# Optimization experiments

Hardware: AMD Instinct MI355X
Metric: run time of the kernel (lower is better)

Reference implementation:

```python
import jax, jax.numpy as jnp
import numpy as np

EMBED_DIM = 128
NUM_SYMBOLS = 200000
PAD = NUM_SYMBOLS
B = 1024          # query batch
FEW = 5           # support set size
NB = 200          # neighbors per entity (fixed by module docstring)
D_MODEL = 2 * EMBED_DIM       # 256
D_INNER = 2 * D_MODEL         # 512
HID = 2 * D_MODEL             # LSTMCell hidden = 2*input_dim = 512
STEPS = 4                     # process_steps
LN_EPS = 1e-5


def setup_inputs() -> dict:
    key = jax.random.key(0)
    ks = jax.random.split(key, 16)

    def conn(k, n):
        c = jax.random.randint(k, (n, NB, 2), 0, NUM_SYMBOLS, dtype=jnp.int64)
        # pad last 50 neighbor slots so the masked max-pool path is exercised
        return c.at[:, 150:, :].set(PAD)

    inp = {
        "query_left_connections": conn(ks[0], B),
        "query_right_connections": conn(ks[1], B),
        "support_left_connections": conn(ks[2], FEW),
        "support_right_connections": conn(ks[3], FEW),
        "query_left_degrees": jax.random.randint(ks[4], (B,), 1, NB, dtype=jnp.int32),
        "query_right_degrees": jax.random.randint(ks[5], (B,), 1, NB, dtype=jnp.int32),
        "support_left_degrees": jax.random.randint(ks[6], (FEW,), 1, NB, dtype=jnp.int32),
        "support_right_degrees": jax.random.randint(ks[7], (FEW,), 1, NB, dtype=jnp.int32),
    }

    # parameters (eval mode: dropout disabled)
    emb = jax.random.normal(ks[8], (NUM_SYMBOLS + 1, EMBED_DIM), jnp.float32) * 0.02
    inp["emb"] = emb.at[PAD].set(0.0)              # padding_idx row is zero
    inp["gcn_W"] = jax.random.normal(ks[9], (EMBED_DIM, 2 * EMBED_DIM), jnp.float32) * 0.05
    inp["gcn_wb"] = jnp.zeros((EMBED_DIM,), jnp.float32)   # gcn_w linear bias
    inp["gcn_b"] = jnp.zeros((EMBED_DIM,), jnp.float32)    # extra gcn_b param (init constant 0)
    inp["proj1_W"] = jax.random.normal(ks[10], (D_INNER, D_MODEL), jnp.float32) * 0.05
    inp["proj1_b"] = jnp.zeros((D_INNER,), jnp.float32)
    inp["proj2_W"] = jax.random.normal(ks[11], (D_MODEL, D_INNER), jnp.float32) * 0.05
    inp["proj2_b"] = jnp.zeros((D_MODEL,), jnp.float32)
    inp["ln_g"] = jnp.ones((D_MODEL,), jnp.float32)
    inp["ln_b"] = jnp.zeros((D_MODEL,), jnp.float32)
    inp["W_ih"] = jax.random.normal(ks[12], (4 * HID, D_MODEL), jnp.float32) * 0.04
    inp["W_hh"] = jax.random.normal(ks[13], (4 * HID, HID), jnp.float32) * 0.04
    inp["b_ih"] = jnp.zeros((4 * HID,), jnp.float32)
    inp["b_hh"] = jnp.zeros((4 * HID,), jnp.float32)
    return inp


def _neighbor_encoder(conn, emb, gcn_W, gcn_wb, gcn_b):
    # conn: (n, NB, 2) ints; gather embed + concat + linear + leaky_relu + masked max + tanh
    rel, ent = conn[:, :, 0], conn[:, :, 1]
    pad_mask = (rel == PAD) | (ent == PAD)                      # (n, NB)
    x = jnp.concatenate([emb[rel], emb[ent]], axis=-1)          # (n, NB, 2E)
    p = jnp.einsum('nke,de->nkd', x, gcn_W) + gcn_wb + gcn_b    # (n, NB, E)
    p = jax.nn.leaky_relu(p, negative_slope=0.1)
    p = jnp.where(pad_mask[:, :, None], -jnp.inf, p)
    return jnp.tanh(jnp.max(p, axis=1))                         # (n, E)


def _support_encoder(x, p1W, p1b, p2W, p2b, g, b):
    # FFN with residual + LayerNorm (GMatching SupportEncoder), dropout off in eval
    h = jax.nn.relu(x @ p1W.T + p1b)
    o = h @ p2W.T + p2b + x
    mu = jnp.mean(o, axis=-1, keepdims=True)
    var = jnp.var(o, axis=-1, keepdims=True)
    return (o - mu) / jnp.sqrt(var + LN_EPS) * g + b


def _query_encoder(support, query, W_ih, W_hh, b_ih, b_hh):
    # GMatching QueryEncoder: LSTMCell attention, `process_steps` iterations
    # support: (1, D_MODEL), query: (bq, D_MODEL)
    bq = query.shape[0]
    h_r = jnp.zeros((bq, HID), query.dtype)
    c = jnp.zeros((bq, HID), query.dtype)
    h = query
    for _ in range(STEPS):
        gates = query @ W_ih.T + b_ih + h_r @ W_hh.T + b_hh     # (bq, 4*HID)
        i, f, g, o = jnp.split(gates, 4, axis=-1)
        c = jax.nn.sigmoid(f) * c + jax.nn.sigmoid(i) * jnp.tanh(g)
        h_new = jax.nn.sigmoid(o) * jnp.tanh(c)                 # (bq, HID)
        h = query + h_new[:, :D_MODEL]
        attn = jax.nn.softmax(h @ support.T, axis=1)            # (bq, 1)
        r = attn @ support                                      # (bq, D_MODEL)
        h_r = jnp.concatenate([h, r], axis=1)
    return h


def reference(query_left_connections, query_right_connections,
              support_left_connections, support_right_connections,
              query_left_degrees, query_right_degrees,
              support_left_degrees, support_right_degrees,
              emb, gcn_W, gcn_wb, gcn_b,
              proj1_W, proj1_b, proj2_W, proj2_b, ln_g, ln_b,
              W_ih, W_hh, b_ih, b_hh):
    ql = _neighbor_encoder(query_left_connections, emb, gcn_W, gcn_wb, gcn_b)
    qr = _neighbor_encoder(query_right_connections, emb, gcn_W, gcn_wb, gcn_b)
    sl = _neighbor_encoder(support_left_connections, emb, gcn_W, gcn_wb, gcn_b)
    sr = _neighbor_encoder(support_right_connections, emb, gcn_W, gcn_wb, gcn_b)
    query_neighbor = jnp.concatenate([ql, qr], axis=-1)      # (B, D_MODEL)
    support_neighbor = jnp.concatenate([sl, sr], axis=-1)    # (FEW, D_MODEL)

    support_g = _support_encoder(support_neighbor[None], proj1_W, proj1_b, proj2_W, proj2_b, ln_g, ln_b)
    support_g = jnp.mean(support_g, axis=1)                  # (1, D_MODEL)
    query_g = _support_encoder(query_neighbor[:, None, :], proj1_W, proj1_b, proj2_W, proj2_b, ln_g, ln_b)
    query_g = query_g[:, 0, :]                               # (B, D_MODEL)

    query_f = _query_encoder(support_g, query_g, W_ih, W_hh, b_ih, b_hh)  # (B, D_MODEL)
    return (query_f @ support_g.T)[:, 0]                     # (B,)
```

## Files before the change

### kernel.cpp

```cpp
#include <hip/hip_runtime.h>
#include <math.h>

#define EMBED   128
#define DMODEL  256
#define DINNER  512
#define HIDN    512
#define NBK     200
#define BQ      1024
#define FEW     5
#define PAD_IDX 200000
#define LN_EPS  1e-5f
#define NTILES  7

#define EMB_ELEMS 25600128
#define EMB_THREADS (EMB_ELEMS / 8)
#define EMB_BLOCKS ((EMB_THREADS + 255) / 256)

typedef short          s16x8  __attribute__((ext_vector_type(8)));
typedef float          f32x4  __attribute__((ext_vector_type(4)));
typedef float          f32x16 __attribute__((ext_vector_type(16)));
typedef unsigned int   u32;
typedef unsigned short u16;

__device__ __forceinline__ float sigmoidf_(float x) { return 1.0f / (1.0f + expf(-x)); }

__device__ __forceinline__ u32 f2bf(float f) {
    u32 u = __builtin_bit_cast(u32, f);
    u += 0x7fffu + ((u >> 16) & 1u);
    return u >> 16;
}
__device__ __forceinline__ s16x8 pack8(float4 a, float4 b) {
    typedef u32 u32x4_ __attribute__((ext_vector_type(4)));
    u32x4_ q;
    q.x = f2bf(a.x) | (f2bf(a.y) << 16);
    q.y = f2bf(a.z) | (f2bf(a.w) << 16);
    q.z = f2bf(b.x) | (f2bf(b.y) << 16);
    q.w = f2bf(b.z) | (f2bf(b.w) << 16);
    return __builtin_bit_cast(s16x8, q);
}

__global__ __launch_bounds__(256) void convert_all_kernel(
    const float* __restrict__ W_ih, const float* __restrict__ W_hh,
    const float* __restrict__ p1W,  const float* __restrict__ p2W,
    const float* __restrict__ emb,
    u16* __restrict__ wih_bf, u16* __restrict__ whh_bf,
    u16* __restrict__ p1_bf,  u16* __restrict__ p2_bf,
    u16* __restrict__ emb_bf)
{
    int bid = blockIdx.x;
    if (bid >= 384) {
        size_t gid = (size_t)(bid - 384) * 256 + threadIdx.x;
        if (gid < EMB_THREADS) {
            size_t base = gid * 8;
            float4 x0 = *(const float4*)(emb + base);
            float4 x1 = *(const float4*)(emb + base + 4);
            *(s16x8*)(emb_bf + base) = pack8(x0, x1);
        }
        return;
    }
    int gid = bid * 256 + threadIdx.x;
    const float* src; u16* dst; int local, stride, KS, liveRemap;
    if (gid < 32768)      { local = gid;          src = W_ih; dst = wih_bf; stride = 256; KS = 8;  liveRemap = 1; }
    else if (gid < 65536) { local = gid - 32768;  src = W_hh; dst = whh_bf; stride = 512; KS = 8;  liveRemap = 1; }
    else if (gid < 81920) { local = gid - 65536;  src = p1W;  dst = p1_bf;  stride = 256; KS = 8;  liveRemap = 0; }
    else                  { local = gid - 81920;  src = p2W;  dst = p2_bf;  stride = 512; KS = 16; liveRemap = 0; }
    int lane = local & 63;
    int ts   = local >> 6;
    int ks   = ts & (KS - 1);
    int tile = ts / KS;
    int n  = tile * 16 + (lane & 15);
    int kb = ks * 32 + (lane >> 4) * 8;
    int row = liveRemap ? ((n >> 8) * 512 + (n & 255)) : n;
    const float* sp = src + (size_t)row * stride + kb;
    float4 x0 = *(const float4*)sp;
    float4 x1 = *(const float4*)(sp + 4);
    *(s16x8*)(dst + (size_t)local * 8) = pack8(x0, x1);
}

template<bool BF>
__global__ __launch_bounds__(256) void neighbor_kernel(
    const int* __restrict__ qlc, const int* __restrict__ qrc,
    const int* __restrict__ slc, const int* __restrict__ src_,
    const float* __restrict__ emb, const u16* __restrict__ emb_bf,
    const float* __restrict__ W,
    const float* __restrict__ wb,  const float* __restrict__ bb,
    float* __restrict__ qn, float* __restrict__ sn)
{
    int b = blockIdx.x;
    const int* conn; float* out; int n; int side;
    if (b < BQ)                { conn = qlc;  n = b;            side = 0; out = qn; }
    else if (b < 2*BQ)         { conn = qrc;  n = b - BQ;       side = 1; out = qn; }
    else if (b < 2*BQ + FEW)   { conn = slc;  n = b - 2*BQ;     side = 0; out = sn; }
    else                       { conn = src_; n = b - 2*BQ-FEW; side = 1; out = sn; }

    int t = threadIdx.x;
    int w = t >> 6, l = t & 63;
    int d0 = w * 32;
    int m31 = l & 31, half = l >> 5;

    s16x8 afrag[16];
    const float* wrow = W + (d0 + m31) * DMODEL + half * 8;
    #pragma unroll
    for (int ks = 0; ks < 16; ++ks) {
        float4 x0 = *(const float4*)(wrow + ks * 16);
        float4 x1 = *(const float4*)(wrow + ks * 16 + 4);
        afrag[ks] = pack8(x0, x1);
    }

    const int2* crow = (const int2*)(conn + n * NBK * 2);
    int srel[NTILES], sent[NTILES];
    u32 vmask = 0;
    #pragma unroll
    for (int nt = 0; nt < NTILES; ++nt) {
        int krow = nt * 32 + m31;
        int rel = PAD_IDX, ent = PAD_IDX;
        if (krow < NBK) { int2 re = crow[krow]; rel = re.x; ent = re.y; }
        int v = (rel != PAD_IDX) && (ent != PAD_IDX);
        if (v) vmask |= (1u << nt);
        srel[nt] = v ? rel : PAD_IDX;
        sent[nt] = v ? ent : PAD_IDX;
    }

    float vm[16];
    #pragma unroll
    for (int r = 0; r < 16; ++r) vm[r] = -INFINITY;

    for (int nt = 0; nt < NTILES; ++nt) {
        if (!__any((int)((vmask >> nt) & 1u))) continue;

        s16x8 bfr[16];
        if (BF) {
            const u16* pr = emb_bf + (size_t)srel[nt] * EMBED + half * 8;
            const u16* pe = emb_bf + (size_t)sent[nt] * EMBED + half * 8;
            #pragma unroll
            for (int ks = 0; ks < 8; ++ks) bfr[ks]     = *(const s16x8*)(pr + ks * 16);
            #pragma unroll
            for (int ks = 0; ks < 8; ++ks) bfr[8 + ks] = *(const s16x8*)(pe + ks * 16);
        } else {
            const float* pr = emb + (size_t)srel[nt] * EMBED + half * 8;
            const float* pe = emb + (size_t)sent[nt] * EMBED + half * 8;
            #pragma unroll
            for (int ks = 0; ks < 8; ++ks)
                bfr[ks] = pack8(*(const float4*)(pr + ks * 16), *(const float4*)(pr + ks * 16 + 4));
            #pragma unroll
            for (int ks = 0; ks < 8; ++ks)
                bfr[8 + ks] = pack8(*(const float4*)(pe + ks * 16), *(const float4*)(pe + ks * 16 + 4));
        }

        f32x16 acc = {0.f,0.f,0.f,0.f,0.f,0.f,0.f,0.f,0.f,0.f,0.f,0.f,0.f,0.f,0.f,0.f};
        #pragma unroll
        for (int j = 0; j < 16; ++j)
            acc = __builtin_amdgcn_mfma_f32_32x32x16_bf16(afrag[j], bfr[j], acc, 0, 0, 0);

        int cv = (vmask >> nt) & 1;
        #pragma unroll
        for (int r = 0; r < 16; ++r) {
            float v = cv ? acc[r] : -INFINITY;
            vm[r] = fmaxf(vm[r], v);
        }
    }

    #pragma unroll
    for (int off = 1; off < 32; off <<= 1) {
        #pragma unroll
        for (int r = 0; r < 16; ++r)
            vm[r] = fmaxf(vm[r], __shfl_xor(vm[r], off, 64));
    }

    if (m31 == 0) {
        #pragma unroll
        for (int r = 0; r < 16; ++r) {
            int d = d0 + (r & 3) + 8 * (r >> 2) + 4 * half;
            float p = vm[r] + wb[d] + bb[d];
            p = (p >= 0.f) ? p : 0.1f * p;
            out[n * DMODEL + side * EMBED + d] = tanhf(p);
        }
    }
}

__global__ __launch_bounds__(512) void support_enc_kernel(
    const float* __restrict__ qn, const float* __restrict__ sn,
    const u16* __restrict__ p1_bf, const float* __restrict__ p1b,
    const u16* __restrict__ p2_bf, const float* __restrict__ p2b,
    const float* __restrict__ lng, const float* __restrict__ lnb,
    float* __restrict__ query_g, float* __restrict__ sup_ln)
{
    __shared__ __align__(16) float xs[16][260];
    __shared__ __align__(16) float hsd[16][516];
    __shared__ __align__(16) float os[16][260];
    int t = threadIdx.x;
    int w = t >> 6, l = t & 63;
    int r0 = blockIdx.x * 16;

    #pragma unroll
    for (int j = 0; j < 8; ++j) {
        int idx = j * 512 + t;
        int r = idx >> 8, cc = idx & 255;
        int row = r0 + r;
        float v = 0.f;
        if (row < BQ + FEW)
            v = (row < BQ) ? qn[(size_t)row * DMODEL + cc] : sn[(size_t)(row - BQ) * DMODEL + cc];
        xs[r][cc] = v;
    }
    __syncthreads();

    int am = l & 15, ak = (l >> 4) * 8;

    s16x8 a1[8];
    #pragma unroll
    for (int ks = 0; ks < 8; ++ks) {
        float4 x0 = *(const float4*)&xs[am][ks * 32 + ak];
        float4 x1 = *(const float4*)&xs[am][ks * 32 + ak + 4];
        a1[ks] = pack8(x0, x1);
    }

    #pragma unroll
    for (int j = 0; j < 4; ++j) {
        int nt = w * 4 + j;
        f32x4 acc = {0.f, 0.f, 0.f, 0.f};
        const u16* bp = p1_bf + (size_t)nt * 4096 + l * 8;
        #pragma unroll
        for (int ks = 0; ks < 8; ++ks) {
            s16x8 bf = *(const s16x8*)(bp + ks * 512);
            acc = __builtin_amdgcn_mfma_f32_16x16x32_bf16(a1[ks], bf, acc, 0, 0, 0);
        }
        int nn = nt * 16 + (l & 15);
        float bj = p1b[nn];
        #pragma unroll
        for (int reg = 0; reg < 4; ++reg) {
            int m = (l >> 4) * 4 + reg;
            hsd[m][nn] = fmaxf(acc[reg] + bj, 0.f);
        }
    }
    __syncthreads();

    s16x8 a2[16];
    #pragma unroll
    for (int ks = 0; ks < 16; ++ks) {
        float4 x0 = *(const float4*)&hsd[am][ks * 32 + ak];
        float4 x1 = *(const float4*)&hsd[am][ks * 32 + ak + 4];
        a2[ks] = pack8(x0, x1);
    }

    #pragma unroll
    for (int j = 0; j < 2; ++j) {
        int nt = w * 2 + j;
        f32x4 acc = {0.f, 0.f, 0.f, 0.f};
        const u16* bp = p2_bf + (size_t)nt * 8192 + l * 8;
        #pragma unroll
        for (int ks = 0; ks < 16; ++ks) {
            s16x8 bf = *(const s16x8*)(bp + ks * 512);
            acc = __builtin_amdgcn_mfma_f32_16x16x32_bf16(a2[ks], bf, acc, 0, 0, 0);
        }
        int nn = nt * 16 + (l & 15);
        float bj = p2b[nn];
        #pragma unroll
        for (int reg = 0; reg < 4; ++reg) {
            int m = (l >> 4) * 4 + reg;
            os[m][nn] = acc[reg] + bj + xs[m][nn];
        }
    }
    __syncthreads();

    for (int j = 0; j < 2; ++j) {
        int m = w * 2 + j;
        float sum = 0.f, sq = 0.f;
        #pragma unroll
        for (int i = 0; i < 4; ++i) {
            float v = os[m][l + 64 * i];
            sum += v; sq += v * v;
        }
        for (int off = 32; off; off >>= 1) {
            sum += __shfl_xor(sum, off, 64);
            sq  += __shfl_xor(sq,  off, 64);
        }
        float mu  = sum * (1.f / DMODEL);
        float var = sq * (1.f / DMODEL) - mu * mu;
        float inv = rsqrtf(var + LN_EPS);
        int row = r0 + m;
        if (row < BQ + FEW) {
            float* outp = (row < BQ) ? (query_g + (size_t)row * DMODEL) : (sup_ln + (size_t)(row - BQ) * DMODEL);
            #pragma unroll
            for (int i = 0; i < 4; ++i) {
                int dd = l + 64 * i;
                outp[dd] = (os[m][dd] - mu) * inv * lng[dd] + lnb[dd];
            }
        }
    }
}

__global__ __launch_bounds__(256) void sWp_kernel(
    const float* __restrict__ sup_ln, const float* __restrict__ W_hh,
    float* __restrict__ sWp)
{
    int w = threadIdx.x >> 6, l = threadIdx.x & 63;
    int wave_id = blockIdx.x * 4 + w;
    float se[4];
    #pragma unroll
    for (int j = 0; j < 4; ++j) {
        float a = 0.f;
        for (int i = 0; i < FEW; ++i) a += sup_ln[i * DMODEL + l + 64 * j];
        se[j] = a * (1.f / FEW);
    }
    for (int i = 0; i < 4; ++i) {
        int p = wave_id * 4 + i;
        int pp = p >> 8, q = p & 255;
        const float* wr = W_hh + (size_t)(pp * 512 + q) * HIDN + 256;
        float part = 0.f;
        #pragma unroll
        for (int j = 0; j < 4; ++j) part += se[j] * wr[l + 64 * j];
        for (int off = 32; off; off >>= 1) part += __shfl_xor(part, off, 64);
        if (l == 0) sWp[p] = part;
    }
}

__global__ __launch_bounds__(512) void lstm_mfma_kernel(
    const float* __restrict__ query_g, const float* __restrict__ sup_ln,
    const float* __restrict__ sWp, const u16* __restrict__ wih_bf,
    const u16* __restrict__ whh_bf, const float* __restrict__ b_ih,
    const float* __restrict__ b_hh, float* __restrict__ out)
{
    __shared__ __align__(16) float qs[16][260];
    __shared__ __align__(16) float hs[16][260];
    __shared__ float sv[DMODEL];
    int t = threadIdx.x;
    int w = t >> 6, l = t & 63;
    int n0 = blockIdx.x * 16;

    if (t < DMODEL) {
        float a = 0.f;
        for (int i = 0; i < FEW; ++i) a += sup_ln[i * DMODEL + t];
        sv[t] = a * (1.f / FEW);
    }
    #pragma unroll
    for (int j = 0; j < 8; ++j) {
        int idx = j * 512 + t;
        int r = idx >> 8, cc = idx & 255;
        qs[r][cc] = query_g[(size_t)(n0 + r) * DMODEL + cc];
    }
    __syncthreads();

    int am = l & 15, ak = (l >> 4) * 8;

    s16x8 af[8];
    #pragma unroll
    for (int ks = 0; ks < 8; ++ks) {
        float4 x0 = *(const float4*)&qs[am][ks * 32 + ak];
        float4 x1 = *(const float4*)&qs[am][ks * 32 + ak + 4];
        af[ks] = pack8(x0, x1);
    }

    f32x4 base[4][2];
    #pragma unroll
    for (int pp = 0; pp < 4; ++pp) {
        #pragma unroll
        for (int qt = 0; qt < 2; ++qt) {
            int tp = pp * 16 + 2 * w + qt;
            f32x4 acc = {0.f, 0.f, 0.f, 0.f};
            const u16* bp = wih_bf + (size_t)tp * 4096 + l * 8;
            #pragma unroll
            for (int ks = 0; ks < 8; ++ks) {
                s16x8 bf = *(const s16x8*)(bp + ks * 512);
                acc = __builtin_amdgcn_mfma_f32_16x16x32_bf16(af[ks], bf, acc, 0, 0, 0);
            }
            base[pp][qt] = acc;
        }
    }
    #pragma unroll
    for (int pp = 0; pp < 4; ++pp) {
        #pragma unroll
        for (int qt = 0; qt < 2; ++qt) {
            int q = w * 32 + qt * 16 + (l & 15);
            float bsv = b_ih[pp * 512 + q] + b_hh[pp * 512 + q];
            base[pp][qt].x += bsv; base[pp][qt].y += bsv;
            base[pp][qt].z += bsv; base[pp][qt].w += bsv;
        }
    }

    float c[2][4];
    #pragma unroll
    for (int qt = 0; qt < 2; ++qt) {
        int q = w * 32 + qt * 16 + (l & 15);
        #pragma unroll
        for (int reg = 0; reg < 4; ++reg) {
            int m = (l >> 4) * 4 + reg;
            float gi = base[0][qt][reg];
            float gg = base[2][qt][reg];
            float go = base[3][qt][reg];
            float cc = sigmoidf_(gi) * tanhf(gg);
            c[qt][reg] = cc;
            hs[m][q] = qs[m][q] + sigmoidf_(go) * tanhf(cc);
        }
    }
    #pragma unroll
    for (int pp = 0; pp < 4; ++pp) {
        #pragma unroll
        for (int qt = 0; qt < 2; ++qt) {
            int q = w * 32 + qt * 16 + (l & 15);
            float sw = sWp[pp * 256 + q];
            base[pp][qt].x += sw; base[pp][qt].y += sw;
            base[pp][qt].z += sw; base[pp][qt].w += sw;
        }
    }
    __syncthreads();

    for (int st = 1; st < 4; ++st) {
        #pragma unroll
        for (int ks = 0; ks < 8; ++ks) {
            float4 x0 = *(const float4*)&hs[am][ks * 32 + ak];
            float4 x1 = *(const float4*)&hs[am][ks * 32 + ak + 4];
            af[ks] = pack8(x0, x1);
        }
        __syncthreads();

        f32x4 gacc[4][2];
        #pragma unroll
        for (int pp = 0; pp < 4; ++pp) {
            #pragma unroll
            for (int qt = 0; qt < 2; ++qt) {
                int tp = pp * 16 + 2 * w + qt;
                f32x4 acc = base[pp][qt];
                const u16* bp = whh_bf + (size_t)tp * 4096 + l * 8;
                #pragma unroll
                for (int ks = 0; ks < 8; ++ks) {
                    s16x8 bf = *(const s16x8*)(bp + ks * 512);
                    acc = __builtin_amdgcn_mfma_f32_16x16x32_bf16(af[ks], bf, acc, 0, 0, 0);
                }
                gacc[pp][qt] = acc;
            }
        }
        #pragma unroll
        for (int qt = 0; qt < 2; ++qt) {
            int q = w * 32 + qt * 16 + (l & 15);
            #pragma unroll
            for (int reg = 0; reg < 4; ++reg) {
                int m = (l >> 4) * 4 + reg;
                float gi = gacc[0][qt][reg];
                float gf = gacc[1][qt][reg];
                float gg = gacc[2][qt][reg];
                float go = gacc[3][qt][reg];
                float cc = sigmoidf_(gf) * c[qt][reg] + sigmoidf_(gi) * tanhf(gg);
                c[qt][reg] = cc;
                hs[m][q] = qs[m][q] + sigmoidf_(go) * tanhf(cc);
            }
        }
        __syncthreads();
    }

    for (int j = 0; j < 2; ++j) {
        int m = w * 2 + j;
        float part = 0.f;
        #pragma unroll
        for (int i = 0; i < 4; ++i) {
            int e = l + 64 * i;
            part += hs[m][e] * sv[e];
        }
        for (int off = 32; off; off >>= 1) part += __shfl_xor(part, off, 64);
        if (l == 0) out[n0 + m] = part;
    }
}

extern "C" void kernel_launch(void* const* d_in, const int* in_sizes, int n_in,
                              void* d_out, int out_size, void* d_ws, size_t ws_size,
                              hipStream_t stream)
{
    const int*   qlc  = (const int*)d_in[0];
    const int*   qrc  = (const int*)d_in[1];
    const int*   slc  = (const int*)d_in[2];
    const int*   src_ = (const int*)d_in[3];
    const float* emb   = (const float*)d_in[8];
    const float* gcnW  = (const float*)d_in[9];
    const float* gcnwb = (const float*)d_in[10];
    const float* gcnb  = (const float*)d_in[11];
    const float* p1W   = (const float*)d_in[12];
    const float* p1b   = (const float*)d_in[13];
    const float* p2W   = (const float*)d_in[14];
    const float* p2b   = (const float*)d_in[15];
    const float* lng   = (const float*)d_in[16];
    const float* lnb   = (const float*)d_in[17];
    const float* W_ih  = (const float*)d_in[18];
    const float* W_hh  = (const float*)d_in[19];
    const float* b_ih  = (const float*)d_in[20];
    const float* b_hh  = (const float*)d_in[21];
    float* out = (float*)d_out;

    char* ws = (char*)d_ws;
    float* qn      = (float*)(ws + 0);
    float* sn      = (float*)(ws + 1048576);
    float* query_g = (float*)(ws + 1053696);
    float* sup_ln  = (float*)(ws + 2102272);
    float* sWp     = (float*)(ws + 2107392);
    u16*   wih_bf  = (u16*)(ws + 2111488);
    u16*   whh_bf  = (u16*)(ws + 2635776);
    u16*   p1_bf   = (u16*)(ws + 3160064);
    u16*   p2_bf   = (u16*)(ws + 3422208);
    u16*   emb_bf  = (u16*)(ws + 3684352);
    (void)in_sizes; (void)n_in; (void)out_size;

    bool have_emb = ws_size >= (size_t)3684352 + (size_t)EMB_ELEMS * 2;
    int grid_conv = 384 + (have_emb ? EMB_BLOCKS : 0);

    convert_all_kernel<<<grid_conv, 256, 0, stream>>>(
        W_ih, W_hh, p1W, p2W, emb, wih_bf, whh_bf, p1_bf, p2_bf, emb_bf);
    if (have_emb)
        neighbor_kernel<true><<<2 * BQ + 2 * FEW, 256, 0, stream>>>(
            qlc, qrc, slc, src_, emb, emb_bf, gcnW, gcnwb, gcnb, qn, sn);
    else
        neighbor_kernel<false><<<2 * BQ + 2 * FEW, 256, 0, stream>>>(
            qlc, qrc, slc, src_, emb, emb_bf, gcnW, gcnwb, gcnb, qn, sn);
    support_enc_kernel<<<(BQ + FEW + 15) / 16, 512, 0, stream>>>(
        qn, sn, p1_bf, p1b, p2_bf, p2b, lng, lnb, query_g, sup_ln);
    sWp_kernel<<<64, 256, 0, stream>>>(sup_ln, W_hh, sWp);
    lstm_mfma_kernel<<<BQ / 16, 512, 0, stream>>>(
        query_g, sup_ln, sWp, wih_bf, whh_bf, b_ih, b_hh, out);
}
```

Before: 404.4 us.

## Stage neighbor embeddings in swizzled LDS and fold support term into LSTM GEMM

In the neighbor kernel, embedding rows are now gathered cooperatively (four threads per row) into a swizzled shared-memory tile, with the next tile prefetched into registers. This replaces per-lane strided gathers that each pulled half-rows. The sWp kernel is removed. The LSTM recurrent GEMM now runs over the full 512-wide hidden input [h, support], with the support vector stored in shared memory and W_hh converted at full width. This drops one launch, but it doubles the recurrent MFMA work and the W_hh conversion, and it adds barriers to the neighbor loop.

```diff
diff --git a/kernel.cpp b/kernel.cpp
--- a/kernel.cpp
+++ b/kernel.cpp
@@ -48,8 +48,8 @@
     u16* __restrict__ emb_bf)
 {
     int bid = blockIdx.x;
-    if (bid >= 384) {
-        size_t gid = (size_t)(bid - 384) * 256 + threadIdx.x;
+    if (bid >= 512) {
+        size_t gid = (size_t)(bid - 512) * 256 + threadIdx.x;
         if (gid < EMB_THREADS) {
             size_t base = gid * 8;
             float4 x0 = *(const float4*)(emb + base);
@@ -60,10 +60,10 @@
     }
     int gid = bid * 256 + threadIdx.x;
     const float* src; u16* dst; int local, stride, KS, liveRemap;
-    if (gid < 32768)      { local = gid;          src = W_ih; dst = wih_bf; stride = 256; KS = 8;  liveRemap = 1; }
-    else if (gid < 65536) { local = gid - 32768;  src = W_hh; dst = whh_bf; stride = 512; KS = 8;  liveRemap = 1; }
-    else if (gid < 81920) { local = gid - 65536;  src = p1W;  dst = p1_bf;  stride = 256; KS = 8;  liveRemap = 0; }
-    else                  { local = gid - 81920;  src = p2W;  dst = p2_bf;  stride = 512; KS = 16; liveRemap = 0; }
+    if (gid < 32768)       { local = gid;          src = W_ih; dst = wih_bf; stride = 256; KS = 8;  liveRemap = 1; }
+    else if (gid < 98304)  { local = gid - 32768;  src = W_hh; dst = whh_bf; stride = 512; KS = 16; liveRemap = 1; }
+    else if (gid < 114688) { local = gid - 98304;  src = p1W;  dst = p1_bf;  stride = 256; KS = 8;  liveRemap = 0; }
+    else                   { local = gid - 114688; src = p2W;  dst = p2_bf;  stride = 512; KS = 16; liveRemap = 0; }
     int lane = local & 63;
     int ts   = local >> 6;
     int ks   = ts & (KS - 1);
@@ -98,6 +98,8 @@
     int d0 = w * 32;
     int m31 = l & 31, half = l >> 5;
 
+    __shared__ __align__(16) u16 bs[64 * 128];
+
     s16x8 afrag[16];
     const float* wrow = W + (d0 + m31) * DMODEL + half * 8;
     #pragma unroll
@@ -108,56 +110,92 @@
     }
 
     const int2* crow = (const int2*)(conn + n * NBK * 2);
-    int srel[NTILES], sent[NTILES];
     u32 vmask = 0;
     #pragma unroll
     for (int nt = 0; nt < NTILES; ++nt) {
         int krow = nt * 32 + m31;
+        if (krow < NBK) {
+            int2 re = crow[krow];
+            if (re.x != PAD_IDX && re.y != PAD_IDX) vmask |= (1u << nt);
+        }
+    }
+
+    int gr = t >> 2, gq = t & 3;
+    int g_m = gr & 31, g_is_ent = gr >> 5;
+    int gsrc[NTILES];
+    #pragma unroll
+    for (int nt = 0; nt < NTILES; ++nt) {
+        int krow = nt * 32 + g_m;
         int rel = PAD_IDX, ent = PAD_IDX;
         if (krow < NBK) { int2 re = crow[krow]; rel = re.x; ent = re.y; }
         int v = (rel != PAD_IDX) && (ent != PAD_IDX);
-        if (v) vmask |= (1u << nt);
-        srel[nt] = v ? rel : PAD_IDX;
-        sent[nt] = v ? ent : PAD_IDX;
-    }
+        gsrc[nt] = v ? (g_is_ent ? ent : rel) : PAD_IDX;
+    }
+
+    int tl[NTILES]; int ntl = 0;
+    #pragma unroll
+    for (int nt = 0; nt < NTILES; ++nt)
+        if (__any((int)((vmask >> nt) & 1u))) tl[ntl++] = nt;
 
     float vm[16];
     #pragma unroll
     for (int r = 0; r < 16; ++r) vm[r] = -INFINITY;
 
-    for (int nt = 0; nt < NTILES; ++nt) {
-        if (!__any((int)((vmask >> nt) & 1u))) continue;
-
-        s16x8 bfr[16];
+    int swl = gr * 128;
+    int rsw_rel = m31 * 128;
+    int rsw_ent = (32 + m31) * 128;
+    int rx = m31 & 15;
+
+    s16x8 stg[4];
+    auto load_tile = [&](int nt, s16x8* dstv) {
         if (BF) {
-            const u16* pr = emb_bf + (size_t)srel[nt] * EMBED + half * 8;
-            const u16* pe = emb_bf + (size_t)sent[nt] * EMBED + half * 8;
+            const u16* p = emb_bf + (size_t)gsrc[nt] * EMBED + gq * 32;
             #pragma unroll
-            for (int ks = 0; ks < 8; ++ks) bfr[ks]     = *(const s16x8*)(pr + ks * 16);
+            for (int i = 0; i < 4; ++i) dstv[i] = *(const s16x8*)(p + i * 8);
+        } else {
+            const float* p = emb + (size_t)gsrc[nt] * EMBED + gq * 32;
             #pragma unroll
-            for (int ks = 0; ks < 8; ++ks) bfr[8 + ks] = *(const s16x8*)(pe + ks * 16);
-        } else {
-            const float* pr = emb + (size_t)srel[nt] * EMBED + half * 8;
-            const float* pe = emb + (size_t)sent[nt] * EMBED + half * 8;
-            #pragma unroll
-            for (int ks = 0; ks < 8; ++ks)
-                bfr[ks] = pack8(*(const float4*)(pr + ks * 16), *(const float4*)(pr + ks * 16 + 4));
-            #pragma unroll
-            for (int ks = 0; ks < 8; ++ks)
-                bfr[8 + ks] = pack8(*(const float4*)(pe + ks * 16), *(const float4*)(pe + ks * 16 + 4));
-        }
+            for (int i = 0; i < 4; ++i)
+                dstv[i] = pack8(*(const float4*)(p + i * 8), *(const float4*)(p + i * 8 + 4));
+        }
+    };
+
+    if (ntl > 0) load_tile(tl[0], stg);
+
+    for (int i = 0; i < ntl; ++i) {
+        int nt = tl[i];
+        __syncthreads();
+        #pragma unroll
+        for (int j = 0; j < 4; ++j) {
+            int c = gq * 4 + j;
+            *(s16x8*)(bs + swl + ((c ^ (gr & 15)) * 8)) = stg[j];
+        }
+        __syncthreads();
+
+        s16x8 stg2[4];
+        if (i + 1 < ntl) load_tile(tl[i + 1], stg2);
 
         f32x16 acc = {0.f,0.f,0.f,0.f,0.f,0.f,0.f,0.f,0.f,0.f,0.f,0.f,0.f,0.f,0.f,0.f};
         #pragma unroll
-        for (int j = 0; j < 16; ++j)
-            acc = __builtin_amdgcn_mfma_f32_32x32x16_bf16(afrag[j], bfr[j], acc, 0, 0, 0);
-
+        for (int ks = 0; ks < 8; ++ks) {
+            int c = ks * 2 + half;
+            s16x8 bfr = *(const s16x8*)(bs + rsw_rel + ((c ^ rx) * 8));
+            acc = __builtin_amdgcn_mfma_f32_32x32x16_bf16(afrag[ks], bfr, acc, 0, 0, 0);
+        }
+        #pragma unroll
+        for (int ks = 0; ks < 8; ++ks) {
+            int c = ks * 2 + half;
+            s16x8 bfr = *(const s16x8*)(bs + rsw_ent + ((c ^ rx) * 8));
+            acc = __builtin_amdgcn_mfma_f32_32x32x16_bf16(afrag[8 + ks], bfr, acc, 0, 0, 0);
+        }
         int cv = (vmask >> nt) & 1;
         #pragma unroll
         for (int r = 0; r < 16; ++r) {
             float v = cv ? acc[r] : -INFINITY;
             vm[r] = fmaxf(vm[r], v);
         }
+        #pragma unroll
+        for (int j = 0; j < 4; ++j) stg[j] = stg2[j];
     }
 
     #pragma unroll
@@ -289,81 +327,58 @@
     }
 }
 
-__global__ __launch_bounds__(256) void sWp_kernel(
-    const float* __restrict__ sup_ln, const float* __restrict__ W_hh,
-    float* __restrict__ sWp)
-{
-    int w = threadIdx.x >> 6, l = threadIdx.x & 63;
-    int wave_id = blockIdx.x * 4 + w;
-    float se[4];
-    #pragma unroll
-    for (int j = 0; j < 4; ++j) {
-        float a = 0.f;
-        for (int i = 0; i < FEW; ++i) a += sup_ln[i * DMODEL + l + 64 * j];
-        se[j] = a * (1.f / FEW);
-    }
-    for (int i = 0; i < 4; ++i) {
-        int p = wave_id * 4 + i;
-        int pp = p >> 8, q = p & 255;
-        const float* wr = W_hh + (size_t)(pp * 512 + q) * HIDN + 256;
-        float part = 0.f;
-        #pragma unroll
-        for (int j = 0; j < 4; ++j) part += se[j] * wr[l + 64 * j];
-        for (int off = 32; off; off >>= 1) part += __shfl_xor(part, off, 64);
-        if (l == 0) sWp[p] = part;
-    }
-}
-
 __global__ __launch_bounds__(512) void lstm_mfma_kernel(
     const float* __restrict__ query_g, const float* __restrict__ sup_ln,
-    const float* __restrict__ sWp, const u16* __restrict__ wih_bf,
-    const u16* __restrict__ whh_bf, const float* __restrict__ b_ih,
-    const float* __restrict__ b_hh, float* __restrict__ out)
+    const u16* __restrict__ wih_bf, const u16* __restrict__ whh_bf,
+    const float* __restrict__ b_ih, const float* __restrict__ b_hh,
+    float* __restrict__ out)
 {
     __shared__ __align__(16) float qs[16][260];
-    __shared__ __align__(16) float hs[16][260];
-    __shared__ float sv[DMODEL];
+    __shared__ __align__(16) float hq[16][516];
     int t = threadIdx.x;
     int w = t >> 6, l = t & 63;
     int n0 = blockIdx.x * 16;
 
-    if (t < DMODEL) {
+    {
+        int cc = t & 255;
         float a = 0.f;
-        for (int i = 0; i < FEW; ++i) a += sup_ln[i * DMODEL + t];
-        sv[t] = a * (1.f / FEW);
-    }
-    #pragma unroll
-    for (int j = 0; j < 8; ++j) {
-        int idx = j * 512 + t;
-        int r = idx >> 8, cc = idx & 255;
-        qs[r][cc] = query_g[(size_t)(n0 + r) * DMODEL + cc];
+        for (int i = 0; i < FEW; ++i) a += sup_ln[i * DMODEL + cc];
+        float svv = a * (1.f / FEW);
+        #pragma unroll
+        for (int j = 0; j < 8; ++j) {
+            int idx = j * 512 + t;
+            int r = idx >> 8;
+            qs[r][cc] = query_g[(size_t)(n0 + r) * DMODEL + cc];
+            hq[r][256 + cc] = svv;
+        }
     }
     __syncthreads();
 
     int am = l & 15, ak = (l >> 4) * 8;
 
-    s16x8 af[8];
-    #pragma unroll
-    for (int ks = 0; ks < 8; ++ks) {
-        float4 x0 = *(const float4*)&qs[am][ks * 32 + ak];
-        float4 x1 = *(const float4*)&qs[am][ks * 32 + ak + 4];
-        af[ks] = pack8(x0, x1);
-    }
-
     f32x4 base[4][2];
-    #pragma unroll
-    for (int pp = 0; pp < 4; ++pp) {
-        #pragma unroll
-        for (int qt = 0; qt < 2; ++qt) {
-            int tp = pp * 16 + 2 * w + qt;
-            f32x4 acc = {0.f, 0.f, 0.f, 0.f};
-            const u16* bp = wih_bf + (size_t)tp * 4096 + l * 8;
+    {
+        s16x8 af[8];
+        #pragma unroll
+        for (int ks = 0; ks < 8; ++ks) {
+            float4 x0 = *(const float4*)&qs[am][ks * 32 + ak];
+            float4 x1 = *(const float4*)&qs[am][ks * 32 + ak + 4];
+            af[ks] = pack8(x0, x1);
+        }
+        #pragma unroll
+        for (int pp = 0; pp < 4; ++pp) {
             #pragma unroll
-            for (int ks = 0; ks < 8; ++ks) {
-                s16x8 bf = *(const s16x8*)(bp + ks * 512);
-                acc = __builtin_amdgcn_mfma_f32_16x16x32_bf16(af[ks], bf, acc, 0, 0, 0);
+            for (int qt = 0; qt < 2; ++qt) {
+                int tp = pp * 16 + 2 * w + qt;
+                f32x4 acc = {0.f, 0.f, 0.f, 0.f};
+                const u16* bp = wih_bf + (size_t)tp * 4096 + l * 8;
+                #pragma unroll
+                for (int ks = 0; ks < 8; ++ks) {
+                    s16x8 bf = *(const s16x8*)(bp + ks * 512);
+                    acc = __builtin_amdgcn_mfma_f32_16x16x32_bf16(af[ks], bf, acc, 0, 0, 0);
+                }
+                base[pp][qt] = acc;
             }
-            base[pp][qt] = acc;
         }
     }
     #pragma unroll
@@ -389,26 +404,17 @@
             float go = base[3][qt][reg];
             float cc = sigmoidf_(gi) * tanhf(gg);
             c[qt][reg] = cc;
-            hs[m][q] = qs[m][q] + sigmoidf_(go) * tanhf(cc);
-        }
-    }
-    #pragma unroll
-    for (int pp = 0; pp < 4; ++pp) {
-        #pragma unroll
-        for (int qt = 0; qt < 2; ++qt) {
-            int q = w * 32 + qt * 16 + (l & 15);
-            float sw = sWp[pp * 256 + q];
-            base[pp][qt].x += sw; base[pp][qt].y += sw;
-            base[pp][qt].z += sw; base[pp][qt].w += sw;
+            hq[m][q] = qs[m][q] + sigmoidf_(go) * tanhf(cc);
         }
     }
     __syncthreads();
 
     for (int st = 1; st < 4; ++st) {
-        #pragma unroll
-        for (int ks = 0; ks < 8; ++ks) {
-            float4 x0 = *(const float4*)&hs[am][ks * 32 + ak];
-            float4 x1 = *(const float4*)&hs[am][ks * 32 + ak + 4];
+        s16x8 af[16];
+        #pragma unroll
+        for (int ks = 0; ks < 16; ++ks) {
+            float4 x0 = *(const float4*)&hq[am][ks * 32 + ak];
+            float4 x1 = *(const float4*)&hq[am][ks * 32 + ak + 4];
             af[ks] = pack8(x0, x1);
         }
         __syncthreads();
@@ -420,9 +426,9 @@
             for (int qt = 0; qt < 2; ++qt) {
                 int tp = pp * 16 + 2 * w + qt;
                 f32x4 acc = base[pp][qt];
-                const u16* bp = whh_bf + (size_t)tp * 4096 + l * 8;
+                const u16* bp = whh_bf + (size_t)tp * 8192 + l * 8;
                 #pragma unroll
-                for (int ks = 0; ks < 8; ++ks) {
+                for (int ks = 0; ks < 16; ++ks) {
                     s16x8 bf = *(const s16x8*)(bp + ks * 512);
                     acc = __builtin_amdgcn_mfma_f32_16x16x32_bf16(af[ks], bf, acc, 0, 0, 0);
                 }
@@ -441,7 +447,7 @@
                 float go = gacc[3][qt][reg];
                 float cc = sigmoidf_(gf) * c[qt][reg] + sigmoidf_(gi) * tanhf(gg);
                 c[qt][reg] = cc;
-                hs[m][q] = qs[m][q] + sigmoidf_(go) * tanhf(cc);
+                hq[m][q] = qs[m][q] + sigmoidf_(go) * tanhf(cc);
             }
         }
         __syncthreads();
@@ -453,7 +459,7 @@
         #pragma unroll
         for (int i = 0; i < 4; ++i) {
             int e = l + 64 * i;
-            part += hs[m][e] * sv[e];
+            part += hq[m][e] * hq[m][256 + e];
         }
         for (int off = 32; off; off >>= 1) part += __shfl_xor(part, off, 64);
         if (l == 0) out[n0 + m] = part;
@@ -489,16 +495,15 @@
     float* sn      = (float*)(ws + 1048576);
     float* query_g = (float*)(ws + 1053696);
     float* sup_ln  = (float*)(ws + 2102272);
-    float* sWp     = (float*)(ws + 2107392);
-    u16*   wih_bf  = (u16*)(ws + 2111488);
-    u16*   whh_bf  = (u16*)(ws + 2635776);
-    u16*   p1_bf   = (u16*)(ws + 3160064);
-    u16*   p2_bf   = (u16*)(ws + 3422208);
-    u16*   emb_bf  = (u16*)(ws + 3684352);
+    u16*   wih_bf  = (u16*)(ws + 2107392);
+    u16*   whh_bf  = (u16*)(ws + 2631680);
+    u16*   p1_bf   = (u16*)(ws + 3680256);
+    u16*   p2_bf   = (u16*)(ws + 3942400);
+    u16*   emb_bf  = (u16*)(ws + 4204544);
     (void)in_sizes; (void)n_in; (void)out_size;
 
-    bool have_emb = ws_size >= (size_t)3684352 + (size_t)EMB_ELEMS * 2;
-    int grid_conv = 384 + (have_emb ? EMB_BLOCKS : 0);
+    bool have_emb = ws_size >= (size_t)4204544 + (size_t)EMB_ELEMS * 2;
+    int grid_conv = 512 + (have_emb ? EMB_BLOCKS : 0);
 
     convert_all_kernel<<<grid_conv, 256, 0, stream>>>(
         W_ih, W_hh, p1W, p2W, emb, wih_bf, whh_bf, p1_bf, p2_bf, emb_bf);
@@ -510,7 +515,6 @@
             qlc, qrc, slc, src_, emb, emb_bf, gcnW, gcnwb, gcnb, qn, sn);
     support_enc_kernel<<<(BQ + FEW + 15) / 16, 512, 0, stream>>>(
         qn, sn, p1_bf, p1b, p2_bf, p2b, lng, lnb, query_g, sup_ln);
-    sWp_kernel<<<64, 256, 0, stream>>>(sup_ln, W_hh, sWp);
     lstm_mfma_kernel<<<BQ / 16, 512, 0, stream>>>(
-        query_g, sup_ln, sWp, wih_bf, whh_bf, b_ih, b_hh, out);
-}
+        query_g, sup_ln, wih_bf, whh_bf, b_ih, b_hh, out);
+}
```

After: 423.4 us. +4.7%, slower.
